# Optimization experiments

Measured on AMD Instinct MI355X. Metric: run time of the kernel, lower is better.

The kernel has to match this reference:

```python
import jax, jax.numpy as jnp
import numpy as np

B, C, H, W = 16, 512, 32, 32
NH = 8
HD = C // NH  # 64


def setup_inputs() -> dict:
    key = jax.random.key(0)
    ks = jax.random.split(key, 9)
    s = 1.0 / np.sqrt(C)
    return {
        "x": jax.random.normal(ks[0], (B, C, H, W), dtype=jnp.float32),
        "Wq": jax.random.normal(ks[1], (C, C), dtype=jnp.float32) * s,
        "bq": jnp.zeros((C,), dtype=jnp.float32),
        "Wk": jax.random.normal(ks[2], (C, C), dtype=jnp.float32) * s,
        "bk": jnp.zeros((C,), dtype=jnp.float32),
        "Wv": jax.random.normal(ks[3], (C, C), dtype=jnp.float32) * s,
        "bv": jnp.zeros((C,), dtype=jnp.float32),
        "Wo": jax.random.normal(ks[4], (C, C), dtype=jnp.float32) * s,
        "bo": jnp.zeros((C,), dtype=jnp.float32),
    }


def reference(x, Wq, bq, Wk, bk, Wv, bv, Wo, bo):
    b, c, h, w = x.shape
    n = h * w  # sequence of spatial tokens
    # [B, C, H, W] -> [B, N, C]
    xf = x.reshape(b, c, n).transpose(0, 2, 1)
    # separate QKV projections, split heads: [B, NH, N, HD]
    def split_heads(t):
        return t.reshape(b, n, NH, HD).transpose(0, 2, 1, 3)
    q = split_heads(xf @ Wq + bq)
    k = split_heads(xf @ Wk + bk)
    v = split_heads(xf @ Wv + bv)
    # energy: [B, NH, N, N]
    energy = jnp.einsum('bhqd,bhkd->bhqk', q, k) / jnp.sqrt(jnp.float32(HD))
    attn = jax.nn.softmax(energy, axis=-1)
    out = jnp.einsum('bhqk,bhkd->bhqd', attn, v)  # [B, NH, N, HD]
    out = out.transpose(0, 2, 1, 3).reshape(b, n, c)
    out = out @ Wo + bo
    return out.transpose(0, 2, 1).reshape(b, c, h, w)
```

## Files before the change

kernel.cpp:

```cpp
#include <hip/hip_runtime.h>
#include <hip/hip_bf16.h>
#include <math.h>

constexpr int B_  = 16;
constexpr int C_  = 512;
constexpr int N_  = 1024;
constexpr int NH_ = 8;
constexpr int HD_ = 64;

#define QSCALE 0.18033688f

typedef __attribute__((ext_vector_type(8))) short short8;
typedef __attribute__((ext_vector_type(4))) short short4v;
typedef __attribute__((ext_vector_type(4))) float f32x4;
#define MFMA16(a, b, c) __builtin_amdgcn_mfma_f32_16x16x32_bf16((a), (b), (c), 0, 0, 0)

#if __has_builtin(__builtin_amdgcn_exp2f)
#define EXP2(x) __builtin_amdgcn_exp2f(x)
#else
#define EXP2(x) exp2f(x)
#endif

__device__ __forceinline__ short f2bf(float f) {
    union { float f; unsigned u; } a; a.f = f;
    unsigned r = a.u + 0x7fffu + ((a.u >> 16) & 1u);
    return (short)(r >> 16);
}
__device__ __forceinline__ short f2bf_hw(float f) {
    __hip_bfloat16 h = __float2bfloat16(f);
    return *reinterpret_cast<short*>(&h);
}

__device__ __forceinline__ void gload_lds16(const void* g, void* l) {
    __builtin_amdgcn_global_load_lds(
        (const __attribute__((address_space(1))) unsigned*)g,
        (__attribute__((address_space(3))) unsigned*)l, 16, 0, 0);
}

__global__ __launch_bounds__(256) void prep_all(
    const float* __restrict__ x, short* __restrict__ xt,
    const float* __restrict__ Wq, const float* __restrict__ Wk,
    const float* __restrict__ Wv, const float* __restrict__ Wo,
    short* __restrict__ WqT, short* __restrict__ WkT,
    short* __restrict__ WvT, short* __restrict__ WoT) {
    __shared__ float t[64][65];
    const int tid = threadIdx.x;
    const int wgid = blockIdx.x;

    const float* src;  short* dst;
    size_t srow0, scol0, drow0, dcol0;
    if (wgid < 2048) {
        const int xcd = wgid & 7;
        const int i = wgid >> 3;
        const int b  = 2 * xcd + (i >= 128);
        const int tile = i & 127;
        const int tn = tile >> 3;
        const int tc = tile & 7;
        src = x;  dst = xt;
        srow0 = (size_t)b * C_ + tc * 64;  scol0 = (size_t)tn * 64;
        drow0 = (size_t)b * N_ + tn * 64;  dcol0 = (size_t)tc * 64;
        #pragma unroll
        for (int k = 0; k < 4; ++k) {
            int s = k * 256 + tid;
            int r = s >> 4, c4 = s & 15;
            float4 v = *(const float4*)&src[(srow0 + r) * N_ + scol0 + c4 * 4];
            *(float4*)&t[r][c4 * 4] = v;
        }
        __syncthreads();
        #pragma unroll
        for (int k = 0; k < 2; ++k) {
            int s = k * 256 + tid;
            int r2 = s >> 3, c8 = s & 7;
            short8 pk;
            #pragma unroll
            for (int j = 0; j < 8; ++j) pk[j] = f2bf(t[c8 * 8 + j][r2]);
            *(short8*)&dst[(drow0 + r2) * C_ + dcol0 + c8 * 8] = pk;
        }
    } else {
        const int idx0 = wgid - 2048;
        const int z = idx0 >> 6;
        src = (z == 0) ? Wq : (z == 1) ? Wk : (z == 2) ? Wv : Wo;
        dst = (z == 0) ? WqT : (z == 1) ? WkT : (z == 2) ? WvT : WoT;
        const int tile = idx0 & 63;
        const int tco = tile >> 3;
        const int tc  = tile & 7;
        srow0 = (size_t)tc * 64;   scol0 = (size_t)tco * 64;
        drow0 = (size_t)tco * 64;  dcol0 = (size_t)tc * 64;
        #pragma unroll
        for (int k = 0; k < 4; ++k) {
            int s = k * 256 + tid;
            int r = s >> 4, c4 = s & 15;
            float4 v = *(const float4*)&src[(srow0 + r) * C_ + scol0 + c4 * 4];
            *(float4*)&t[r][c4 * 4] = v;
        }
        __syncthreads();
        #pragma unroll
        for (int k = 0; k < 2; ++k) {
            int s = k * 256 + tid;
            int r2 = s >> 3, c8 = s & 7;
            short8 pk;
            #pragma unroll
            for (int j = 0; j < 8; ++j) pk[j] = f2bf(t[c8 * 8 + j][r2]);
            *(short8*)&dst[(drow0 + r2) * C_ + dcol0 + c8 * 8] = pk;
        }
    }
}

#define GEMM_STAGE(buf, t)                                                    \
    {                                                                         \
        _Pragma("unroll")                                                     \
        for (int ii = 0; ii < 4; ++ii) {                                      \
            gload_lds16(Ag + arowoff + (size_t)ii * 8 * C_ + (t) * 64,        \
                        &smem[buf][0][wave * 32 + ii * 8][0]);                \
            gload_lds16(Bg + arowoff + (size_t)ii * 8 * C_ + (t) * 64,        \
                        &smem[buf][1][wave * 32 + ii * 8][0]);                \
        }                                                                     \
    }

#define GEMM_CORE()                                                           \
    GEMM_STAGE(0, 0);                                                         \
    __syncthreads();                                                          \
    for (int t = 0; t < 8; ++t) {                                             \
        const int buf = t & 1;                                                \
        if (t < 7) GEMM_STAGE(buf ^ 1, t + 1);                                \
        __builtin_amdgcn_s_setprio(1);                                        \
        _Pragma("unroll")                                                     \
        for (int ks = 0; ks < 2; ++ks) {                                      \
            short8 af[4], bf[4];                                              \
            const int sw = ((ks * 4 + g) ^ (c & 7)) << 3;                     \
            _Pragma("unroll")                                                 \
            for (int fm = 0; fm < 4; ++fm)                                    \
                af[fm] = *(const short8*)&smem[buf][0][wm * 64 + fm * 16 + c][sw]; \
            _Pragma("unroll")                                                 \
            for (int fn = 0; fn < 4; ++fn)                                    \
                bf[fn] = *(const short8*)&smem[buf][1][wn * 64 + fn * 16 + c][sw]; \
            _Pragma("unroll")                                                 \
            for (int fm = 0; fm < 4; ++fm)                                    \
                _Pragma("unroll")                                             \
                for (int fn = 0; fn < 4; ++fn)                                \
                    acc[fm][fn] = MFMA16(af[fm], bf[fn], acc[fm][fn]);        \
        }                                                                     \
        __builtin_amdgcn_s_setprio(0);                                        \
        __syncthreads();                                                      \
    }

__global__ __launch_bounds__(256) void qkv_mfma(
    const short* __restrict__ xt,
    const short* __restrict__ WqT, const float* __restrict__ bq,
    const short* __restrict__ WkT, const float* __restrict__ bk,
    const short* __restrict__ WvT, const float* __restrict__ bv,
    short* __restrict__ Qs, short* __restrict__ Kb, short* __restrict__ Vt) {
    const int wgid = blockIdx.x;
    const int xcd = wgid & 7;
    const int i = wgid >> 3;
    const int b = 2 * xcd + (i >= 96);
    const int rem = (i >= 96) ? i - 96 : i;
    const int z = rem >> 5;
    const int tile = rem & 31;
    const int mt = tile >> 2;
    const int nt = tile & 3;
    const int tid = threadIdx.x;
    const int wave = tid >> 6, lane = tid & 63;
    const int g = lane >> 4, c = lane & 15;
    const int wm = wave >> 1, wn = wave & 1;

    const short* W    = (z == 0) ? WqT : (z == 1) ? WkT : WvT;
    const float* bias = (z == 0) ? bq  : (z == 1) ? bk  : bv;

    __shared__ __align__(16) short smem[2][2][128][64];

    const short* Ag = xt + (size_t)b * N_ * C_ + (size_t)mt * 128 * C_;
    const short* Bg = W + (size_t)nt * 128 * C_;

    const int lrow = lane >> 3, lslot = lane & 7;
    const size_t arowoff = (size_t)(wave * 32 + lrow) * C_ + ((lslot ^ lrow) << 3);

    f32x4 acc[4][4] = {};
    GEMM_CORE();

    const int tok0 = mt * 128 + wm * 64;
    const int co0  = nt * 128 + wn * 64;
    const int h = co0 >> 6;
    const size_t bh = (size_t)(b * NH_ + h);

    if (z < 2) {
        short* Y = (z == 0) ? Qs : Kb;
        const float sc = (z == 0) ? QSCALE : 1.f;
        #pragma unroll
        for (int fm = 0; fm < 4; ++fm)
            #pragma unroll
            for (int fn = 0; fn < 4; ++fn)
                #pragma unroll
                for (int r = 0; r < 4; ++r) {
                    int tok = tok0 + fm * 16 + 4 * g + r;
                    int hd  = fn * 16 + c;
                    float v = (acc[fm][fn][r] + bias[co0 + hd]) * sc;
                    Y[(bh * N_ + tok) * HD_ + hd] = f2bf_hw(v);
                }
    } else {
        short (*t72)[72] = (short(*)[72])((short*)smem + wave * 32 * 72);
        #pragma unroll
        for (int p = 0; p < 2; ++p) {
            #pragma unroll
            for (int fn2 = 0; fn2 < 2; ++fn2) {
                int fnn = 2 * p + fn2;
                #pragma unroll
                for (int fm = 0; fm < 4; ++fm) {
                    short4v pk;
                    #pragma unroll
                    for (int r = 0; r < 4; ++r)
                        pk[r] = f2bf_hw(acc[fm][fnn][r] + bias[co0 + fnn * 16 + c]);
                    *(short4v*)&t72[fn2 * 16 + c][fm * 16 + 4 * g] = pk;
                }
            }
            int row = lane >> 1, half2 = lane & 1;
            int hd = p * 32 + row;
            size_t base = (bh * HD_ + hd) * N_ + tok0 + half2 * 32;
            #pragma unroll
            for (int j = 0; j < 4; ++j)
                *(short8*)&Vt[base + j * 8] = *(const short8*)&t72[row][half2 * 32 + j * 8];
        }
    }
}

__global__ __launch_bounds__(512) void attn_mfma(
    const short* __restrict__ Qs, const short* __restrict__ Kb,
    const short* __restrict__ Vt, short* __restrict__ Ah) {
    const int wgid = blockIdx.x;
    const int swz  = (wgid & 7) * 64 + (wgid >> 3);
    const int b  = swz >> 5;
    const int h  = (swz >> 2) & 7;
    const int qt = swz & 3;
    const int tid = threadIdx.x;
    const int wave = tid >> 6, lane = tid & 63;
    const int g = lane >> 4, c = lane & 15;
    const int q0 = qt * 256 + wave * 32;
    const size_t bh = (size_t)(b * NH_ + h);

    const short* Qw  = Qs + (bh * N_ + q0) * HD_;
    const short* Kbb = Kb + bh * N_ * HD_;
    const short* Vtb = Vt + bh * HD_ * N_;

    __shared__ short KV[2][2][4096];
    __shared__ short Pl[8][32][64];
    short (*P)[64] = Pl[wave];
    const int px = (c & 7) << 1;

    const int srow = tid >> 3;
    const int sc16 = tid & 7;
    const int kdst = srow * 64 + 8 * (sc16 ^ (srow & 7));
    short8 gk, gv;

    #define STAGE_LOAD(key0)                                                   \
        do {                                                                   \
            gk = *(const short8*)&Kbb[(size_t)((key0) + srow) * HD_ + sc16 * 8]; \
            gv = *(const short8*)&Vtb[(size_t)srow * N_ + (key0) + sc16 * 8];    \
        } while (0)
    #define STAGE_WRITE(buf)                                                   \
        do {                                                                   \
            *(short8*)&KV[buf][0][kdst] = gk;                                  \
            *(short8*)&KV[buf][1][kdst] = gv;                                  \
        } while (0)

    short8 qf[2][2];
    #pragma unroll
    for (int f = 0; f < 2; ++f)
        #pragma unroll
        for (int k0 = 0; k0 < 2; ++k0)
            qf[f][k0] = *(const short8*)&Qw[(f * 16 + c) * HD_ + k0 * 32 + g * 8];

    short8 ones8;
    #pragma unroll
    for (int j = 0; j < 8; ++j) ones8[j] = (short)0x3F80;

    f32x4 o[2][4] = {};
    f32x4 lacc[2] = {};

    STAGE_LOAD(0);
    STAGE_WRITE(0);
    STAGE_LOAD(64);
    __syncthreads();

    int cur = 0;
    for (int it = 0; it < 16; ++it) {
        if (it < 15) STAGE_WRITE(cur ^ 1);
        if (it < 14) STAGE_LOAD((it + 2) * 64);

        const short* Kl = &KV[cur][0][0];
        const short* Vl = &KV[cur][1][0];

        f32x4 s[2][4] = {};
        __builtin_amdgcn_s_setprio(1);
        #pragma unroll
        for (int m = 0; m < 4; ++m) {
            const int row = m * 16 + c;
            short8 ka = *(const short8*)&Kl[row * 64 + 8 * ((g)     ^ (row & 7))];
            short8 kb = *(const short8*)&Kl[row * 64 + 8 * ((4 + g) ^ (row & 7))];
            s[0][m] = MFMA16(ka, qf[0][0], s[0][m]);
            s[0][m] = MFMA16(kb, qf[0][1], s[0][m]);
            s[1][m] = MFMA16(ka, qf[1][0], s[1][m]);
            s[1][m] = MFMA16(kb, qf[1][1], s[1][m]);
        }
        __builtin_amdgcn_s_setprio(0);

        #pragma unroll
        for (int f = 0; f < 2; ++f) {
            #pragma unroll
            for (int m = 0; m < 4; ++m) {
                short4v pk;
                #pragma unroll
                for (int r = 0; r < 4; ++r) pk[r] = f2bf_hw(EXP2(s[f][m][r]));
                *(short4v*)&P[f * 16 + c][((4 * m + g) ^ px) * 4] = pk;
            }
        }

        short8 pa[2][2];
        #pragma unroll
        for (int f = 0; f < 2; ++f)
            #pragma unroll
            for (int k0 = 0; k0 < 2; ++k0)
                pa[f][k0] = *(const short8*)&P[f * 16 + c][((k0 * 8 + 2 * g) ^ px) * 4];
        __builtin_amdgcn_s_setprio(1);
        lacc[0] = MFMA16(pa[0][0], ones8, lacc[0]);
        lacc[0] = MFMA16(pa[0][1], ones8, lacc[0]);
        lacc[1] = MFMA16(pa[1][0], ones8, lacc[1]);
        lacc[1] = MFMA16(pa[1][1], ones8, lacc[1]);
        #pragma unroll
        for (int n = 0; n < 4; ++n) {
            const int row = n * 16 + c;
            short8 va = *(const short8*)&Vl[row * 64 + 8 * ((g)     ^ (row & 7))];
            short8 vb = *(const short8*)&Vl[row * 64 + 8 * ((4 + g) ^ (row & 7))];
            o[0][n] = MFMA16(pa[0][0], va, o[0][n]);
            o[0][n] = MFMA16(pa[0][1], vb, o[0][n]);
            o[1][n] = MFMA16(pa[1][0], va, o[1][n]);
            o[1][n] = MFMA16(pa[1][1], vb, o[1][n]);
        }
        __builtin_amdgcn_s_setprio(0);

        __syncthreads();
        cur ^= 1;
    }
    #undef STAGE_LOAD
    #undef STAGE_WRITE

    #pragma unroll
    for (int f = 0; f < 2; ++f) {
        float li[4];
        #pragma unroll
        for (int r = 0; r < 4; ++r) li[r] = 1.f / lacc[f][r];
        #pragma unroll
        for (int n = 0; n < 4; ++n)
            #pragma unroll
            for (int r = 0; r < 4; ++r) {
                int tok = q0 + f * 16 + 4 * g + r;
                int cc  = h * 64 + n * 16 + c;
                Ah[((size_t)b * N_ + tok) * C_ + cc] = f2bf_hw(o[f][n][r] * li[r]);
            }
    }
}

__global__ __launch_bounds__(256) void proj_mfma(
    const short* __restrict__ Ah, const short* __restrict__ WoT,
    const float* __restrict__ bo, float* __restrict__ out) {
    const int wgid = blockIdx.x;
    const int xcd = wgid & 7;
    const int i = wgid >> 3;
    const int b = 2 * xcd + (i >= 32);
    const int tile = i & 31;
    const int mt = tile >> 2;
    const int nt = tile & 3;
    const int tid = threadIdx.x;
    const int wave = tid >> 6, lane = tid & 63;
    const int g = lane >> 4, c = lane & 15;
    const int wm = wave >> 1, wn = wave & 1;

    __shared__ __align__(16) short smem[2][2][128][64];

    const short* Ag = Ah + (size_t)b * N_ * C_ + (size_t)mt * 128 * C_;
    const short* Bg = WoT + (size_t)nt * 128 * C_;

    const int lrow = lane >> 3, lslot = lane & 7;
    const size_t arowoff = (size_t)(wave * 32 + lrow) * C_ + ((lslot ^ lrow) << 3);

    f32x4 acc[4][4] = {};
    GEMM_CORE();

    const int tok0 = mt * 128 + wm * 64;
    const int co0  = nt * 128 + wn * 64;

    float (*tf)[68] = (float(*)[68])((float*)smem + wave * 32 * 68);
    #pragma unroll
    for (int p = 0; p < 2; ++p) {
        #pragma unroll
        for (int fm = 0; fm < 4; ++fm)
            #pragma unroll
            for (int fn2 = 0; fn2 < 2; ++fn2) {
                float4 v = *(float4*)&acc[fm][2 * p + fn2];
                *(float4*)&tf[fn2 * 16 + c][fm * 16 + 4 * g] = v;
            }
        int row = lane >> 1, half = lane & 1;
        int co = co0 + p * 32 + row;
        float bias = bo[co];
        float* ob = out + ((size_t)b * C_ + co) * N_ + tok0 + half * 32;
        #pragma unroll
        for (int j = 0; j < 8; ++j) {
            float4 v = *(const float4*)&tf[row][half * 32 + j * 4];
            v.x += bias; v.y += bias; v.z += bias; v.w += bias;
            *(float4*)&ob[j * 4] = v;
        }
    }
}

extern "C" void kernel_launch(void* const* d_in, const int* in_sizes, int n_in,
                              void* d_out, int out_size, void* d_ws, size_t ws_size,
                              hipStream_t stream) {
    (void)in_sizes; (void)n_in; (void)out_size; (void)ws_size;
    const float* x  = (const float*)d_in[0];
    const float* Wq = (const float*)d_in[1];
    const float* bq = (const float*)d_in[2];
    const float* Wk = (const float*)d_in[3];
    const float* bk = (const float*)d_in[4];
    const float* Wv = (const float*)d_in[5];
    const float* bv = (const float*)d_in[6];
    const float* Wo = (const float*)d_in[7];
    const float* bo = (const float*)d_in[8];
    float* out = (float*)d_out;

    char* ws = (char*)d_ws;
    const size_t MB = 1024 * 1024;
    short* xt  = (short*)(ws + 0 * MB);
    short* WqT = (short*)(ws + 16 * MB);
    short* WkT = (short*)(ws + 16 * MB + 512 * 1024);
    short* WvT = (short*)(ws + 17 * MB);
    short* WoT = (short*)(ws + 17 * MB + 512 * 1024);
    short* Qsb = (short*)(ws + 18 * MB);
    short* Kb  = (short*)(ws + 34 * MB);
    short* Vt  = (short*)(ws + 50 * MB);
    short* Ah  = (short*)(ws + 66 * MB);

    prep_all<<<dim3(2304), 256, 0, stream>>>(x, xt, Wq, Wk, Wv, Wo,
                                             WqT, WkT, WvT, WoT);
    qkv_mfma<<<dim3(1536), 256, 0, stream>>>(xt, WqT, bq, WkT, bk, WvT, bv,
                                             Qsb, Kb, Vt);
    attn_mfma<<<dim3(512), 512, 0, stream>>>(Qsb, Kb, Vt, Ah);
    proj_mfma<<<dim3(512), 256, 0, stream>>>(Ah, WoT, bo, out);
}
```

Baseline: 108.3 us.

## Switch attention to 32x32 MFMA with register-resident P via permlane swaps

```diff
diff --git a/kernel.cpp b/kernel.cpp
--- a/kernel.cpp
+++ b/kernel.cpp
@@ -13,7 +13,10 @@
 typedef __attribute__((ext_vector_type(8))) short short8;
 typedef __attribute__((ext_vector_type(4))) short short4v;
 typedef __attribute__((ext_vector_type(4))) float f32x4;
+typedef __attribute__((ext_vector_type(16))) float f32x16;
+typedef __attribute__((ext_vector_type(2))) int int2v;
 #define MFMA16(a, b, c) __builtin_amdgcn_mfma_f32_16x16x32_bf16((a), (b), (c), 0, 0, 0)
+#define MFMA32(a, b, c) __builtin_amdgcn_mfma_f32_32x32x16_bf16((a), (b), (c), 0, 0, 0)
 
 #if __has_builtin(__builtin_amdgcn_exp2f)
 #define EXP2(x) __builtin_amdgcn_exp2f(x)
@@ -29,6 +32,21 @@
 __device__ __forceinline__ short f2bf_hw(float f) {
     __hip_bfloat16 h = __float2bfloat16(f);
     return *reinterpret_cast<short*>(&h);
+}
+__device__ __forceinline__ unsigned pk2(float a, float b) {
+    return (unsigned)(unsigned short)f2bf_hw(a) |
+           ((unsigned)(unsigned short)f2bf_hw(b) << 16);
+}
+
+__device__ __forceinline__ void swap32(unsigned a, unsigned b,
+                                       unsigned &d, unsigned &s2, int hi) {
+#if __has_builtin(__builtin_amdgcn_permlane32_swap)
+    int2v p = __builtin_amdgcn_permlane32_swap((int)a, (int)b, false, false);
+    d = (unsigned)p[0]; s2 = (unsigned)p[1];
+#else
+    d  = hi ? (unsigned)__shfl_xor((int)b, 32) : a;
+    s2 = hi ? b : (unsigned)__shfl_xor((int)a, 32);
+#endif
 }
 
 __device__ __forceinline__ void gload_lds16(const void* g, void* l) {
@@ -233,7 +251,7 @@
     const int qt = swz & 3;
     const int tid = threadIdx.x;
     const int wave = tid >> 6, lane = tid & 63;
-    const int g = lane >> 4, c = lane & 15;
+    const int ql = lane & 31, hi = lane >> 5;
     const int q0 = qt * 256 + wave * 32;
     const size_t bh = (size_t)(b * NH_ + h);
 
@@ -242,9 +260,6 @@
     const short* Vtb = Vt + bh * HD_ * N_;
 
     __shared__ short KV[2][2][4096];
-    __shared__ short Pl[8][32][64];
-    short (*P)[64] = Pl[wave];
-    const int px = (c & 7) << 1;
 
     const int srow = tid >> 3;
     const int sc16 = tid & 7;
@@ -262,19 +277,13 @@
             *(short8*)&KV[buf][1][kdst] = gv;                                  \
         } while (0)
 
-    short8 qf[2][2];
+    short8 qf[4];
     #pragma unroll
-    for (int f = 0; f < 2; ++f)
-        #pragma unroll
-        for (int k0 = 0; k0 < 2; ++k0)
-            qf[f][k0] = *(const short8*)&Qw[(f * 16 + c) * HD_ + k0 * 32 + g * 8];
-
-    short8 ones8;
-    #pragma unroll
-    for (int j = 0; j < 8; ++j) ones8[j] = (short)0x3F80;
-
-    f32x4 o[2][4] = {};
-    f32x4 lacc[2] = {};
+    for (int ks = 0; ks < 4; ++ks)
+        qf[ks] = *(const short8*)&Qw[ql * HD_ + ks * 16 + hi * 8];
+
+    f32x16 o0 = {}, o1 = {};
+    float l_run = 0.f;
 
     STAGE_LOAD(0);
     STAGE_WRITE(0);
@@ -289,51 +298,63 @@
         const short* Kl = &KV[cur][0][0];
         const short* Vl = &KV[cur][1][0];
 
-        f32x4 s[2][4] = {};
+        f32x16 s0 = {}, s1 = {};
         __builtin_amdgcn_s_setprio(1);
         #pragma unroll
-        for (int m = 0; m < 4; ++m) {
-            const int row = m * 16 + c;
-            short8 ka = *(const short8*)&Kl[row * 64 + 8 * ((g)     ^ (row & 7))];
-            short8 kb = *(const short8*)&Kl[row * 64 + 8 * ((4 + g) ^ (row & 7))];
-            s[0][m] = MFMA16(ka, qf[0][0], s[0][m]);
-            s[0][m] = MFMA16(kb, qf[0][1], s[0][m]);
-            s[1][m] = MFMA16(ka, qf[1][0], s[1][m]);
-            s[1][m] = MFMA16(kb, qf[1][1], s[1][m]);
+        for (int ks = 0; ks < 4; ++ks) {
+            const int sl = 8 * (((ks << 1) + hi) ^ (ql & 7));
+            short8 k0f = *(const short8*)&Kl[ql * 64 + sl];
+            short8 k1f = *(const short8*)&Kl[(32 + ql) * 64 + sl];
+            s0 = MFMA32(k0f, qf[ks], s0);
+            s1 = MFMA32(k1f, qf[ks], s1);
         }
         __builtin_amdgcn_s_setprio(0);
 
         #pragma unroll
-        for (int f = 0; f < 2; ++f) {
-            #pragma unroll
-            for (int m = 0; m < 4; ++m) {
-                short4v pk;
-                #pragma unroll
-                for (int r = 0; r < 4; ++r) pk[r] = f2bf_hw(EXP2(s[f][m][r]));
-                *(short4v*)&P[f * 16 + c][((4 * m + g) ^ px) * 4] = pk;
-            }
-        }
-
-        short8 pa[2][2];
-        #pragma unroll
-        for (int f = 0; f < 2; ++f)
-            #pragma unroll
-            for (int k0 = 0; k0 < 2; ++k0)
-                pa[f][k0] = *(const short8*)&P[f * 16 + c][((k0 * 8 + 2 * g) ^ px) * 4];
+        for (int r = 0; r < 16; ++r) s0[r] = EXP2(s0[r]);
+        #pragma unroll
+        for (int r = 0; r < 16; ++r) s1[r] = EXP2(s1[r]);
+        {
+            float a8[8];
+            #pragma unroll
+            for (int r = 0; r < 8; ++r)
+                a8[r] = (s0[r] + s0[r + 8]) + (s1[r] + s1[r + 8]);
+            l_run += ((a8[0] + a8[1]) + (a8[2] + a8[3])) +
+                     ((a8[4] + a8[5]) + (a8[6] + a8[7]));
+        }
+
+        unsigned w0[4][2], w1[4][2];
+        #pragma unroll
+        for (int t4 = 0; t4 < 4; ++t4) {
+            w0[t4][0] = pk2(s0[4 * t4 + 0], s0[4 * t4 + 1]);
+            w0[t4][1] = pk2(s0[4 * t4 + 2], s0[4 * t4 + 3]);
+            w1[t4][0] = pk2(s1[4 * t4 + 0], s1[4 * t4 + 1]);
+            w1[t4][1] = pk2(s1[4 * t4 + 2], s1[4 * t4 + 3]);
+        }
+        short8 pf[4];
+        #pragma unroll
+        for (int ks = 0; ks < 4; ++ks) {
+            const int e = 2 * (ks & 1);
+            unsigned a0 = (ks < 2) ? w0[e][0]     : w1[e][0];
+            unsigned b0 = (ks < 2) ? w0[e + 1][0] : w1[e + 1][0];
+            unsigned a1 = (ks < 2) ? w0[e][1]     : w1[e][1];
+            unsigned b1 = (ks < 2) ? w0[e + 1][1] : w1[e + 1][1];
+            unsigned d0, s20, d1, s21;
+            swap32(a0, b0, d0, s20, hi);
+            swap32(a1, b1, d1, s21, hi);
+            int4 fw;
+            fw.x = (int)d0; fw.y = (int)d1; fw.z = (int)s20; fw.w = (int)s21;
+            pf[ks] = *(short8*)&fw;
+        }
+
         __builtin_amdgcn_s_setprio(1);
-        lacc[0] = MFMA16(pa[0][0], ones8, lacc[0]);
-        lacc[0] = MFMA16(pa[0][1], ones8, lacc[0]);
-        lacc[1] = MFMA16(pa[1][0], ones8, lacc[1]);
-        lacc[1] = MFMA16(pa[1][1], ones8, lacc[1]);
-        #pragma unroll
-        for (int n = 0; n < 4; ++n) {
-            const int row = n * 16 + c;
-            short8 va = *(const short8*)&Vl[row * 64 + 8 * ((g)     ^ (row & 7))];
-            short8 vb = *(const short8*)&Vl[row * 64 + 8 * ((4 + g) ^ (row & 7))];
-            o[0][n] = MFMA16(pa[0][0], va, o[0][n]);
-            o[0][n] = MFMA16(pa[0][1], vb, o[0][n]);
-            o[1][n] = MFMA16(pa[1][0], va, o[1][n]);
-            o[1][n] = MFMA16(pa[1][1], vb, o[1][n]);
+        #pragma unroll
+        for (int ks = 0; ks < 4; ++ks) {
+            const int sl = 8 * (((ks << 1) + hi) ^ (ql & 7));
+            short8 v0f = *(const short8*)&Vl[ql * 64 + sl];
+            short8 v1f = *(const short8*)&Vl[(32 + ql) * 64 + sl];
+            o0 = MFMA32(v0f, pf[ks], o0);
+            o1 = MFMA32(v1f, pf[ks], o1);
         }
         __builtin_amdgcn_s_setprio(0);
 
@@ -343,19 +364,28 @@
     #undef STAGE_LOAD
     #undef STAGE_WRITE
 
+    float l = l_run;
+#if __has_builtin(__builtin_amdgcn_permlane32_swap)
+    {
+        int2v p = __builtin_amdgcn_permlane32_swap(__float_as_int(l),
+                                                   __float_as_int(l), false, false);
+        l = __int_as_float(p[0]) + __int_as_float(p[1]);
+    }
+#else
+    l += __shfl_xor(l, 32);
+#endif
+    const float li = 1.f / l;
+    short* Arow = Ah + ((size_t)b * N_ + q0 + ql) * C_ + h * 64;
     #pragma unroll
-    for (int f = 0; f < 2; ++f) {
-        float li[4];
-        #pragma unroll
-        for (int r = 0; r < 4; ++r) li[r] = 1.f / lacc[f][r];
-        #pragma unroll
-        for (int n = 0; n < 4; ++n)
-            #pragma unroll
-            for (int r = 0; r < 4; ++r) {
-                int tok = q0 + f * 16 + 4 * g + r;
-                int cc  = h * 64 + n * 16 + c;
-                Ah[((size_t)b * N_ + tok) * C_ + cc] = f2bf_hw(o[f][n][r] * li[r]);
-            }
+    for (int t = 0; t < 4; ++t) {
+        short4v pa, pb;
+        #pragma unroll
+        for (int j = 0; j < 4; ++j) {
+            pa[j] = f2bf_hw(o0[4 * t + j] * li);
+            pb[j] = f2bf_hw(o1[4 * t + j] * li);
+        }
+        *(short4v*)&Arow[8 * t + 4 * hi]      = pa;
+        *(short4v*)&Arow[32 + 8 * t + 4 * hi] = pb;
     }
 }
 
```

New measurement: 116.2 us. +7.3%, slower.
